# Kernel optimization log

Hardware: AMD Instinct MI355X
Metric: run time of the kernel (lower is better)

## Reference

```python
import jax, jax.numpy as jnp
import numpy as np

NH = 16      # num_attention_heads
NKV = 8      # num_key_value_heads
G = NH // NKV  # num_key_value_groups
D = 128      # head_dim = hidden_size // NH
ROPE_MAX = 2048


def _rope_tables(seq_len, dtype=jnp.float32):
    # matches RotaryEmbedding: inv_freq over even dims, freqs duplicated (concat), cos/sin cached
    inv_freq = 1.0 / (10000.0 ** (jnp.arange(0, D, 2, dtype=jnp.float32) / D))
    t = jnp.arange(ROPE_MAX, dtype=jnp.float32)[:, None]          # [max, 1]
    freqs = t * inv_freq[None, :]                                  # [max, D/2]
    freqs = jnp.concatenate((freqs, freqs), axis=-1)               # [max, D]
    cos = jnp.cos(freqs)[:seq_len].astype(dtype)                   # [S, D]
    sin = jnp.sin(freqs)[:seq_len].astype(dtype)
    # unsqueeze(0) then unsqueeze(2) -> [1, S, 1, D] broadcasting over batch and heads
    return cos[None, :, None, :], sin[None, :, None, :]


def _rotate_half(x):
    x1, x2 = jnp.split(x, 2, axis=-1)
    return jnp.concatenate((-x2, x1), axis=-1)


def setup_inputs() -> dict:
    key = jax.random.key(0)
    ks = jax.random.split(key, 5)
    B, S, H = 2, 2048, 2048
    scale = 1.0 / np.sqrt(H)
    return {
        "hidden_states": jax.random.normal(ks[0], (B, S, H), jnp.float32),
        "Wq": jax.random.normal(ks[1], (H, H), jnp.float32) * scale,
        "Wk": jax.random.normal(ks[2], (NKV * D, H), jnp.float32) * scale,
        "Wv": jax.random.normal(ks[3], (NKV * D, H), jnp.float32) * scale,
        "Wo": jax.random.normal(ks[4], (H, H), jnp.float32) * scale,
    }


def reference(hidden_states, Wq, Wk, Wv, Wo):
    B, S, H = hidden_states.shape
    # projections (nn.Linear: y = x @ W.T, no bias)
    q = (hidden_states @ Wq.T).reshape(B, S, NH, D)     # [B,S,NH,D]
    k = (hidden_states @ Wk.T).reshape(B, S, NKV, D)    # [B,S,NKV,D]
    v = (hidden_states @ Wv.T).reshape(B, S, NKV, D)

    cos, sin = _rope_tables(S, hidden_states.dtype)
    q = q * cos + _rotate_half(q) * sin
    k = k * cos + _rotate_half(k) * sin

    # GQA: query head h attends to kv head h // G (repeat_kv ordering: h = n*G + g)
    qg = q.reshape(B, S, NKV, G, D).transpose(0, 2, 3, 1, 4)   # [B,NKV,G,S,D]
    kt = k.transpose(0, 2, 1, 3)                                # [B,NKV,S,D]
    vt = v.transpose(0, 2, 1, 3)                                # [B,NKV,S,D]

    scores = jnp.einsum("bngqd,bnkd->bngqk", qg, kt) / np.sqrt(D)  # [B,NKV,G,S,S]
    causal = jnp.triu(jnp.ones((S, S), dtype=bool), k=1)
    neg = jnp.finfo(scores.dtype).min
    scores = jnp.where(causal[None, None, None], neg, scores)
    probs = jax.nn.softmax(scores.astype(jnp.float32), axis=-1).astype(q.dtype)

    out = jnp.einsum("bngqk,bnkd->bngqd", probs, vt)            # [B,NKV,G,S,D]
    out = out.transpose(0, 3, 1, 2, 4).reshape(B, S, H)         # [B,S,H]
    return out @ Wo.T
```

## Files before the change

### kernel.cpp

```cpp
#include <hip/hip_runtime.h>

typedef unsigned short u16;
typedef __attribute__((ext_vector_type(8))) short short8;
typedef __attribute__((ext_vector_type(4))) float f32x4;

__device__ __forceinline__ u16 f2bf(float f) {
  unsigned u = __float_as_uint(f);
  return (u16)((u + 0x7FFFu + ((u >> 16) & 1u)) >> 16);
}
__device__ __forceinline__ float bf2f(u16 h) {
  return __uint_as_float(((unsigned)h) << 16);
}

__device__ __forceinline__ void gload_lds16(const void* g, void* l) {
  __builtin_amdgcn_global_load_lds(
      (const __attribute__((address_space(1))) unsigned*)g,
      (__attribute__((address_space(3))) unsigned*)l, 16, 0, 0);
}

__global__ void cast_f32_bf16_k(const float4* __restrict__ in, u16* __restrict__ out, int n4) {
  int i = blockIdx.x * 256 + threadIdx.x;
  if (i >= n4) return;
  float4 v = in[i];
  union { u16 u[4]; uint2 d; } r;
  r.u[0] = f2bf(v.x); r.u[1] = f2bf(v.y); r.u[2] = f2bf(v.z); r.u[3] = f2bf(v.w);
  *reinterpret_cast<uint2*>(out + (size_t)i * 4) = r.d;
}

__global__ void rope_tables_k(float* __restrict__ cosT, float* __restrict__ sinT) {
  int idx = blockIdx.x * 256 + threadIdx.x;
  int i = idx & 63, s = idx >> 6;
  double inv = pow(10000.0, -(double)(2 * i) / 128.0);
  double f = (double)s * inv;
  cosT[idx] = (float)cos(f);
  sinT[idx] = (float)sin(f);
}

__global__ void rope_q_k(u16* __restrict__ x, const float* __restrict__ cosT,
                         const float* __restrict__ sinT) {
  int idx = blockIdx.x * 256 + threadIdx.x;
  int i = idx & 63;
  int hh = (idx >> 6) & 15;
  int row = idx >> 10;
  int s = row & 2047;
  size_t base = (size_t)row * 4096 + hh * 128;
  float x1 = bf2f(x[base + i]);
  float x2 = bf2f(x[base + i + 64]);
  float c = cosT[s * 64 + i], sn = sinT[s * 64 + i];
  x[base + i]      = f2bf(x1 * c - x2 * sn);
  x[base + i + 64] = f2bf(x2 * c + x1 * sn);
}

__global__ void rope_repack_k_k(const u16* __restrict__ qkv, u16* __restrict__ kt,
                                const float* __restrict__ cosT, const float* __restrict__ sinT) {
  int idx = blockIdx.x * 256 + threadIdx.x;
  int i = idx & 63;
  int kvh = (idx >> 6) & 7;
  int row = idx >> 9;
  int s = row & 2047, b = row >> 11;
  size_t src = (size_t)row * 4096 + 2048 + kvh * 128;
  float x1 = bf2f(qkv[src + i]);
  float x2 = bf2f(qkv[src + i + 64]);
  float c = cosT[s * 64 + i], sn = sinT[s * 64 + i];
  size_t dst = ((size_t)(b * 8 + kvh) * 2048 + s) * 128;
  kt[dst + i]      = f2bf(x1 * c - x2 * sn);
  kt[dst + i + 64] = f2bf(x2 * c + x1 * sn);
}

__global__ void transpose_v_k(const u16* __restrict__ qkv, u16* __restrict__ vt) {
  __shared__ u16 tile[128][129];
  int bn = blockIdx.y;
  int s0 = blockIdx.x * 128;
  int b = bn >> 3, n = bn & 7;
  for (int e = threadIdx.x; e < 128 * 128; e += 256) {
    int r = e >> 7, c = e & 127;
    tile[r][c] = qkv[(size_t)(b * 2048 + s0 + r) * 4096 + 3072 + n * 128 + c];
  }
  __syncthreads();
  for (int e = threadIdx.x; e < 128 * 128; e += 256) {
    int r = e >> 7, c = e & 127;
    vt[((size_t)bn * 128 + r) * 2048 + s0 + c] = tile[c][r];
  }
}

template<typename OutT>
__global__ __launch_bounds__(512, 1) void gemm256p_k(
    const u16* __restrict__ A, const u16* __restrict__ Bm,
    OutT* __restrict__ C, int M, int N, int K)
{
  __shared__ __align__(16) u16 As[2][2][256 * 32];
  __shared__ __align__(16) u16 Bs[2][2][256 * 32];
  const int tid = threadIdx.x;
  const int wave = tid >> 6, lane = tid & 63;
  const int wm = wave >> 2, wn = wave & 3;
  const int lrow = lane & 15, lgrp = lane >> 4;
  const int gx = (int)gridDim.x;
  const int nwg = gx * (int)gridDim.y;
  const int f = (int)(blockIdx.y * gridDim.x + blockIdx.x);
  const int sw = (f & 7) * (nwg >> 3) + (f >> 3);
  const int bx = sw % gx, by = sw / gx;
  const int row0 = by * 256, col0 = bx * 256;

  f32x4 acc[8][4];
  #pragma unroll
  for (int m = 0; m < 8; ++m)
    #pragma unroll
    for (int n = 0; n < 4; ++n) acc[m][n] = (f32x4){0.f, 0.f, 0.f, 0.f};

  const int NT = K >> 6;
  const int psw = lgrp ^ (lrow & 3);

  auto stageA = [&](int buf, int t, int ks) {
    const int k0 = (t << 6) + ks * 32;
    #pragma unroll
    for (int i = 0; i < 2; ++i) {
      int s = i * 512 + tid;
      int row = s >> 2, p = s & 3;
      int g = p ^ (row & 3);
      gload_lds16(A + (size_t)(row0 + row) * K + k0 + g * 8,
                  &As[buf][ks][(size_t)(i * 512 + wave * 64) * 8]);
    }
  };
  auto stageB = [&](int buf, int t, int ks) {
    const int k0 = (t << 6) + ks * 32;
    #pragma unroll
    for (int i = 0; i < 2; ++i) {
      int s = i * 512 + tid;
      int row = s >> 2, p = s & 3;
      int g = p ^ (row & 3);
      gload_lds16(Bm + (size_t)(col0 + row) * K + k0 + g * 8,
                  &Bs[buf][ks][(size_t)(i * 512 + wave * 64) * 8]);
    }
  };

  stageA(0, 0, 0); stageB(0, 0, 0); stageA(0, 0, 1); stageB(0, 0, 1);

  for (int t = 0; t < NT; ++t) {
    const int cur = t & 1, nxt = cur ^ 1;
    const bool pf = (t + 1 < NT);
    short8 af[4], bfr[4];

    if (pf) { stageA(nxt, t + 1, 0); asm volatile("s_waitcnt vmcnt(6)" ::: "memory"); }
    else    {                        asm volatile("s_waitcnt vmcnt(4)" ::: "memory"); }
    __builtin_amdgcn_s_barrier();
    __builtin_amdgcn_sched_barrier(0);
    #pragma unroll
    for (int m = 0; m < 4; ++m)
      af[m] = *reinterpret_cast<const short8*>(&As[cur][0][(wm * 128 + m * 16 + lrow) * 32 + psw * 8]);
    #pragma unroll
    for (int n = 0; n < 4; ++n)
      bfr[n] = *reinterpret_cast<const short8*>(&Bs[cur][0][(wn * 64 + n * 16 + lrow) * 32 + psw * 8]);
    asm volatile("s_waitcnt lgkmcnt(0)" ::: "memory");
    __builtin_amdgcn_sched_barrier(0);
    __builtin_amdgcn_s_setprio(1);
    #pragma unroll
    for (int m = 0; m < 4; ++m)
      #pragma unroll
      for (int n = 0; n < 4; ++n)
        acc[m][n] = __builtin_amdgcn_mfma_f32_16x16x32_bf16(af[m], bfr[n], acc[m][n], 0, 0, 0);
    __builtin_amdgcn_s_setprio(0);

    if (pf) stageB(nxt, t + 1, 0);
    #pragma unroll
    for (int m = 0; m < 4; ++m)
      af[m] = *reinterpret_cast<const short8*>(&As[cur][0][(wm * 128 + (m + 4) * 16 + lrow) * 32 + psw * 8]);
    asm volatile("s_waitcnt lgkmcnt(0)" ::: "memory");
    __builtin_amdgcn_sched_barrier(0);
    __builtin_amdgcn_s_setprio(1);
    #pragma unroll
    for (int m = 0; m < 4; ++m)
      #pragma unroll
      for (int n = 0; n < 4; ++n)
        acc[m + 4][n] = __builtin_amdgcn_mfma_f32_16x16x32_bf16(af[m], bfr[n], acc[m + 4][n], 0, 0, 0);
    __builtin_amdgcn_s_setprio(0);

    if (pf) { stageA(nxt, t + 1, 1); asm volatile("s_waitcnt vmcnt(6)" ::: "memory"); }
    else    {                        asm volatile("s_waitcnt vmcnt(0)" ::: "memory"); }
    __builtin_amdgcn_s_barrier();
    __builtin_amdgcn_sched_barrier(0);
    #pragma unroll
    for (int m = 0; m < 4; ++m)
      af[m] = *reinterpret_cast<const short8*>(&As[cur][1][(wm * 128 + m * 16 + lrow) * 32 + psw * 8]);
    #pragma unroll
    for (int n = 0; n < 4; ++n)
      bfr[n] = *reinterpret_cast<const short8*>(&Bs[cur][1][(wn * 64 + n * 16 + lrow) * 32 + psw * 8]);
    asm volatile("s_waitcnt lgkmcnt(0)" ::: "memory");
    __builtin_amdgcn_sched_barrier(0);
    __builtin_amdgcn_s_setprio(1);
    #pragma unroll
    for (int m = 0; m < 4; ++m)
      #pragma unroll
      for (int n = 0; n < 4; ++n)
        acc[m][n] = __builtin_amdgcn_mfma_f32_16x16x32_bf16(af[m], bfr[n], acc[m][n], 0, 0, 0);
    __builtin_amdgcn_s_setprio(0);

    if (pf) stageB(nxt, t + 1, 1);
    #pragma unroll
    for (int m = 0; m < 4; ++m)
      af[m] = *reinterpret_cast<const short8*>(&As[cur][1][(wm * 128 + (m + 4) * 16 + lrow) * 32 + psw * 8]);
    asm volatile("s_waitcnt lgkmcnt(0)" ::: "memory");
    __builtin_amdgcn_sched_barrier(0);
    __builtin_amdgcn_s_setprio(1);
    #pragma unroll
    for (int m = 0; m < 4; ++m)
      #pragma unroll
      for (int n = 0; n < 4; ++n)
        acc[m + 4][n] = __builtin_amdgcn_mfma_f32_16x16x32_bf16(af[m], bfr[n], acc[m + 4][n], 0, 0, 0);
    __builtin_amdgcn_s_setprio(0);
  }

  #pragma unroll
  for (int m = 0; m < 8; ++m)
    #pragma unroll
    for (int n = 0; n < 4; ++n)
      #pragma unroll
      for (int j = 0; j < 4; ++j) {
        int r = row0 + wm * 128 + m * 16 + lgrp * 4 + j;
        int col = col0 + wn * 64 + n * 16 + lrow;
        float val = acc[m][n][j];
        if constexpr (sizeof(OutT) == 2) C[(size_t)r * N + col] = f2bf(val);
        else                             C[(size_t)r * N + col] = val;
      }
}

template<typename OutT, int BN>
__global__ __launch_bounds__(512, 1) void gemm256_k(
    const u16* __restrict__ A, const u16* __restrict__ Bm,
    OutT* __restrict__ C, int M, int N, int K)
{
  constexpr int BITER = (BN * 8) / 512;
  constexpr int NFR = BN / 64;
  __shared__ __align__(16) u16 As[2][256 * 64];
  __shared__ __align__(16) u16 Bs[2][BN * 64];
  const int tid = threadIdx.x;
  const int wave = tid >> 6, lane = tid & 63;
  const int wm = wave >> 2, wn = wave & 3;
  const int lrow = lane & 15, lgrp = lane >> 4;
  const int gx = (int)gridDim.x;
  const int nwg = gx * (int)gridDim.y;
  const int f = (int)(blockIdx.y * gridDim.x + blockIdx.x);
  const int sw = (f & 7) * (nwg >> 3) + (f >> 3);
  const int bx = sw % gx, by = sw / gx;
  const int row0 = by * 256, col0 = bx * BN;

  f32x4 acc[8][NFR];
  #pragma unroll
  for (int m = 0; m < 8; ++m)
    #pragma unroll
    for (int n = 0; n < NFR; ++n) acc[m][n] = (f32x4){0.f, 0.f, 0.f, 0.f};

  const int NT = K >> 6;

  auto stage = [&](int buf, int k0) {
    #pragma unroll
    for (int i = 0; i < 4; ++i) {
      int cid = i * 512 + tid;
      int row = cid >> 3, cp = cid & 7;
      int c = cp ^ (row & 7);
      gload_lds16(A + (size_t)(row0 + row) * K + k0 + c * 8,
                  &As[buf][(size_t)(i * 512 + wave * 64) * 8]);
    }
    #pragma unroll
    for (int i = 0; i < BITER; ++i) {
      int cid = i * 512 + tid;
      int row = cid >> 3, cp = cid & 7;
      int c = cp ^ (row & 7);
      gload_lds16(Bm + (size_t)(col0 + row) * K + k0 + c * 8,
                  &Bs[buf][(size_t)(i * 512 + wave * 64) * 8]);
    }
  };

  stage(0, 0);
  for (int t = 0; t < NT; ++t) {
    const int cur = t & 1;
    if (t + 1 < NT) {
      stage(cur ^ 1, (t + 1) << 6);
      if constexpr (BN == 256) asm volatile("s_waitcnt vmcnt(8)" ::: "memory");
      else                     asm volatile("s_waitcnt vmcnt(6)" ::: "memory");
    } else {
      asm volatile("s_waitcnt vmcnt(0)" ::: "memory");
    }
    __builtin_amdgcn_s_barrier();
    __builtin_amdgcn_sched_barrier(0);
    #pragma unroll
    for (int ks = 0; ks < 2; ++ks) {
      short8 af[8], bfr[NFR];
      #pragma unroll
      for (int m = 0; m < 8; ++m) {
        int row = wm * 128 + m * 16 + lrow;
        int cp = (ks * 4 + lgrp) ^ (row & 7);
        af[m] = *reinterpret_cast<const short8*>(&As[cur][row * 64 + cp * 8]);
      }
      #pragma unroll
      for (int n = 0; n < NFR; ++n) {
        int row = wn * (NFR * 16) + n * 16 + lrow;
        int cp = (ks * 4 + lgrp) ^ (row & 7);
        bfr[n] = *reinterpret_cast<const short8*>(&Bs[cur][row * 64 + cp * 8]);
      }
      #pragma unroll
      for (int m = 0; m < 8; ++m)
        #pragma unroll
        for (int n = 0; n < NFR; ++n)
          acc[m][n] = __builtin_amdgcn_mfma_f32_16x16x32_bf16(af[m], bfr[n], acc[m][n], 0, 0, 0);
    }
    __builtin_amdgcn_sched_barrier(0);
    __builtin_amdgcn_s_barrier();
  }

  #pragma unroll
  for (int m = 0; m < 8; ++m)
    #pragma unroll
    for (int n = 0; n < NFR; ++n)
      #pragma unroll
      for (int j = 0; j < 4; ++j) {
        int r = row0 + wm * 128 + m * 16 + lgrp * 4 + j;
        int col = col0 + wn * (NFR * 16) + n * 16 + lrow;
        float val = acc[m][n][j];
        if constexpr (sizeof(OutT) == 2) C[(size_t)r * N + col] = f2bf(val);
        else                             C[(size_t)r * N + col] = val;
      }
}

__global__ __launch_bounds__(256, 2) void flash_attn_k(
    const u16* __restrict__ qkv, const u16* __restrict__ kt,
    const u16* __restrict__ vt, u16* __restrict__ o)
{
  constexpr int S = 2048, NH = 16, NKV = 8, D = 128;
  const int wave = threadIdx.x >> 6, lane = threadIdx.x & 63;
  const int flat = blockIdx.x;
  const int pr = flat >> 5;
  const int bh = (flat & 7) * 4 + ((flat >> 3) & 3);
  const int b = bh >> 4, h = bh & 15;
  const int kvh = h >> 1;
  const int lrow = lane & 15, lgrp = lane >> 4;

  __shared__ __align__(16) u16 ks[2][64 * 128];
  __shared__ __align__(16) u16 vs[2][128 * 64];

  const float scl2 = 0.12754245006443634f;
  const u16* khead = kt + (size_t)(b * NKV + kvh) * S * D;
  const u16* vhead = vt + (size_t)(b * NKV + kvh) * D * S;

  auto stage = [&](int nxt, int kv0n) {
    #pragma unroll
    for (int i = 0; i < 4; ++i) {
      int c = i * 256 + wave * 64 + lane;
      int kr = c >> 4;
      int kc16 = (c & 15) ^ (kr & 7);
      gload_lds16(khead + (size_t)(kv0n + kr) * D + kc16 * 8,
                  &ks[nxt][(size_t)(i * 256 + wave * 64) * 8]);
      int vr = c >> 3;
      int vc = (c & 7) ^ (vr & 7);
      gload_lds16(vhead + (size_t)vr * S + kv0n + vc * 8,
                  &vs[nxt][(size_t)(i * 256 + wave * 64) * 8]);
    }
  };

  #pragma unroll
  for (int ph = 0; ph < 2; ++ph) {
    const int qt = ph ? pr : (31 - pr);
    const int q0 = qt * 64 + wave * 16;
    const int trips = qt + 1;

    short8 qf[4];
    const u16* qbase = qkv + (size_t)(b * S + q0 + lrow) * 4096 + h * 128;
    #pragma unroll
    for (int kc = 0; kc < 4; ++kc)
      qf[kc] = *reinterpret_cast<const short8*>(qbase + kc * 32 + lgrp * 8);

    f32x4 acc[8];
    #pragma unroll
    for (int n = 0; n < 8; ++n) acc[n] = (f32x4){0.f, 0.f, 0.f, 0.f};
    float l_part[4] = {0.f, 0.f, 0.f, 0.f};

    stage(0, 0);
    __syncthreads();

    for (int t = 0; t < trips; ++t) {
      const int cur = t & 1;
      const int kv0 = t * 64;
      f32x4 sc[4];
      #pragma unroll
      for (int nb = 0; nb < 4; ++nb) {
        sc[nb] = (f32x4){0.f, 0.f, 0.f, 0.f};
        const int r = nb * 16 + lrow;
        #pragma unroll
        for (int kc = 0; kc < 4; ++kc) {
          int ch = (kc * 4 + lgrp) ^ (r & 7);
          short8 kf = *reinterpret_cast<const short8*>(&ks[cur][r * 128 + ch * 8]);
          sc[nb] = __builtin_amdgcn_mfma_f32_16x16x32_bf16(qf[kc], kf, sc[nb], 0, 0, 0);
        }
      }
      __syncthreads();
      if (t + 1 < trips) stage(cur ^ 1, kv0 + 64);
      u16* pb = &ks[cur][wave * 1024];
      if (t < trips - 1) {
        #pragma unroll
        for (int nb = 0; nb < 4; ++nb)
          #pragma unroll
          for (int j = 0; j < 4; ++j) {
            int qr = lgrp * 4 + j;
            float p = exp2f(fminf(sc[nb][j] * scl2, 43.f));
            l_part[j] += p;
            pb[qr * 64 + ((nb * 16 + lrow) ^ ((qr & 7) << 3))] = f2bf(p);
          }
      } else {
        #pragma unroll
        for (int nb = 0; nb < 4; ++nb) {
          if (nb < wave) {
            #pragma unroll
            for (int j = 0; j < 4; ++j) {
              int qr = lgrp * 4 + j;
              float p = exp2f(fminf(sc[nb][j] * scl2, 43.f));
              l_part[j] += p;
              pb[qr * 64 + ((nb * 16 + lrow) ^ ((qr & 7) << 3))] = f2bf(p);
            }
          } else if (nb == wave) {
            #pragma unroll
            for (int j = 0; j < 4; ++j) {
              int qr = lgrp * 4 + j;
              float p = (lrow <= qr) ? exp2f(fminf(sc[nb][j] * scl2, 43.f)) : 0.f;
              l_part[j] += p;
              pb[qr * 64 + ((nb * 16 + lrow) ^ ((qr & 7) << 3))] = f2bf(p);
            }
          } else {
            #pragma unroll
            for (int j = 0; j < 4; ++j) {
              int qr = lgrp * 4 + j;
              pb[qr * 64 + ((nb * 16 + lrow) ^ ((qr & 7) << 3))] = 0;
            }
          }
        }
      }
      short8 pf[2];
      #pragma unroll
      for (int kc2 = 0; kc2 < 2; ++kc2) {
        int ch = (kc2 * 4 + lgrp) ^ (lrow & 7);
        pf[kc2] = *reinterpret_cast<const short8*>(&pb[lrow * 64 + ch * 8]);
      }
      #pragma unroll
      for (int n = 0; n < 8; ++n) {
        const int d = n * 16 + lrow;
        #pragma unroll
        for (int kc2 = 0; kc2 < 2; ++kc2) {
          int ch = (kc2 * 4 + lgrp) ^ (d & 7);
          short8 vf = *reinterpret_cast<const short8*>(&vs[cur][d * 64 + ch * 8]);
          acc[n] = __builtin_amdgcn_mfma_f32_16x16x32_bf16(pf[kc2], vf, acc[n], 0, 0, 0);
        }
      }
      __syncthreads();
    }

    float inv[4];
    #pragma unroll
    for (int j = 0; j < 4; ++j) {
      float s = l_part[j];
      #pragma unroll
      for (int off = 8; off; off >>= 1) s += __shfl_xor(s, off);
      inv[j] = 1.f / s;
    }
    u16* obase = o + (((size_t)(b * S + q0)) * NH + h) * D;
    #pragma unroll
    for (int n = 0; n < 8; ++n)
      #pragma unroll
      for (int j = 0; j < 4; ++j)
        obase[(size_t)(lgrp * 4 + j) * NH * D + n * 16 + lrow] = f2bf(acc[n][j] * inv[j]);
    __syncthreads();
  }
}

extern "C" void kernel_launch(void* const* d_in, const int* in_sizes, int n_in,
                              void* d_out, int out_size, void* d_ws, size_t ws_size,
                              hipStream_t stream) {
  const float* hs = (const float*)d_in[0];
  const float* Wq = (const float*)d_in[1];
  const float* Wk = (const float*)d_in[2];
  const float* Wv = (const float*)d_in[3];
  const float* Wo = (const float*)d_in[4];
  float* out = (float*)d_out;

  constexpr int B = 2, S = 2048, H = 2048, NH = 16, NKV = 8, D = 128;
  constexpr int M = B * S;
  constexpr int NQKV = 4096;

  char* w = (char*)d_ws;
  auto alloc = [&](size_t bytes) { char* p = w; w += (bytes + 255) & ~(size_t)255; return p; };
  u16* hs_bf   = (u16*)alloc((size_t)M * H * 2);
  u16* wqkv_bf = (u16*)alloc((size_t)NQKV * H * 2);
  u16* wo_bf   = (u16*)alloc((size_t)H * H * 2);
  u16* qkv     = (u16*)alloc((size_t)M * NQKV * 2);
  float* cosT  = (float*)alloc((size_t)S * 64 * 4);
  float* sinT  = (float*)alloc((size_t)S * 64 * 4);
  u16* attn = hs_bf;
  u16* vt   = wqkv_bf;
  u16* kt   = wqkv_bf + (size_t)B * NKV * D * S;

  cast_f32_bf16_k<<<(M * H / 4) / 256, 256, 0, stream>>>((const float4*)hs, hs_bf, M * H / 4);
  cast_f32_bf16_k<<<(H * H / 4) / 256, 256, 0, stream>>>((const float4*)Wq, wqkv_bf, H * H / 4);
  cast_f32_bf16_k<<<(NKV * D * H / 4) / 256, 256, 0, stream>>>((const float4*)Wk, wqkv_bf + (size_t)2048 * H, NKV * D * H / 4);
  cast_f32_bf16_k<<<(NKV * D * H / 4) / 256, 256, 0, stream>>>((const float4*)Wv, wqkv_bf + (size_t)3072 * H, NKV * D * H / 4);
  cast_f32_bf16_k<<<(H * H / 4) / 256, 256, 0, stream>>>((const float4*)Wo, wo_bf, H * H / 4);
  rope_tables_k<<<(S * 64) / 256, 256, 0, stream>>>(cosT, sinT);

  gemm256p_k<u16><<<dim3(NQKV / 256, M / 256), 512, 0, stream>>>(hs_bf, wqkv_bf, qkv, M, NQKV, H);

  rope_q_k<<<(M * 16 * 64) / 256, 256, 0, stream>>>(qkv, cosT, sinT);
  rope_repack_k_k<<<(M * 8 * 64) / 256, 256, 0, stream>>>(qkv, kt, cosT, sinT);
  transpose_v_k<<<dim3(S / 128, B * NKV), 256, 0, stream>>>(qkv, vt);

  flash_attn_k<<<512, 256, 0, stream>>>(qkv, kt, vt, attn);

  gemm256_k<float, 128><<<dim3(H / 128, M / 256), 512, 0, stream>>>(attn, wo_bf, out, M, H, H);
}
```

Measured before the change: 234.5 us.

## Keep attention probabilities in registers via transposed MFMA and lane shuffles

The attention kernel swaps the MFMA operand order so each lane holds a column of scores. The softmax probabilities are packed to bf16 with v_cvt_pk_bf16 and redistributed to the P·V operand layout with cross-lane shuffles, which removes the LDS write/read round trip of P. It also cuts one of the two per-tile barriers by using an explicit vmcnt wait plus s_barrier, and writes outputs as packed 8-byte stores. In exchange it adds 16 shuffles per tile and depends on correctly reasoning about the register layout and the reuse of the K buffer.

```diff
diff --git a/kernel.cpp b/kernel.cpp
--- a/kernel.cpp
+++ b/kernel.cpp
@@ -10,6 +10,11 @@
 }
 __device__ __forceinline__ float bf2f(u16 h) {
   return __uint_as_float(((unsigned)h) << 16);
+}
+__device__ __forceinline__ unsigned cvt_pk_bf16(float lo, float hi) {
+  unsigned r;
+  asm("v_cvt_pk_bf16_f32 %0, %1, %2" : "=v"(r) : "v"(lo), "v"(hi));
+  return r;
 }
 
 __device__ __forceinline__ void gload_lds16(const void* g, void* l) {
@@ -341,6 +346,10 @@
   const u16* khead = kt + (size_t)(b * NKV + kvh) * S * D;
   const u16* vhead = vt + (size_t)(b * NKV + kvh) * D * S;
 
+  const int srcA = lrow + 16 * ((2 * lgrp) & 3);
+  const int srcB = srcA + 16;
+  const bool hiSel = (lgrp >= 2);
+
   auto stage = [&](int nxt, int kv0n) {
     #pragma unroll
     for (int i = 0; i < 4; ++i) {
@@ -371,14 +380,15 @@
     f32x4 acc[8];
     #pragma unroll
     for (int n = 0; n < 8; ++n) acc[n] = (f32x4){0.f, 0.f, 0.f, 0.f};
-    float l_part[4] = {0.f, 0.f, 0.f, 0.f};
+    float l_part = 0.f;
 
     stage(0, 0);
-    __syncthreads();
 
     for (int t = 0; t < trips; ++t) {
       const int cur = t & 1;
-      const int kv0 = t * 64;
+      asm volatile("s_waitcnt vmcnt(0)" ::: "memory");
+      __builtin_amdgcn_s_barrier();
+      __builtin_amdgcn_sched_barrier(0);
       f32x4 sc[4];
       #pragma unroll
       for (int nb = 0; nb < 4; ++nb) {
@@ -388,55 +398,57 @@
         for (int kc = 0; kc < 4; ++kc) {
           int ch = (kc * 4 + lgrp) ^ (r & 7);
           short8 kf = *reinterpret_cast<const short8*>(&ks[cur][r * 128 + ch * 8]);
-          sc[nb] = __builtin_amdgcn_mfma_f32_16x16x32_bf16(qf[kc], kf, sc[nb], 0, 0, 0);
+          sc[nb] = __builtin_amdgcn_mfma_f32_16x16x32_bf16(kf, qf[kc], sc[nb], 0, 0, 0);
         }
       }
-      __syncthreads();
-      if (t + 1 < trips) stage(cur ^ 1, kv0 + 64);
-      u16* pb = &ks[cur][wave * 1024];
+      if (t + 1 < trips) stage(cur ^ 1, (t + 1) * 64);
+      float p[4][4];
       if (t < trips - 1) {
         #pragma unroll
         for (int nb = 0; nb < 4; ++nb)
           #pragma unroll
-          for (int j = 0; j < 4; ++j) {
-            int qr = lgrp * 4 + j;
-            float p = exp2f(fminf(sc[nb][j] * scl2, 43.f));
-            l_part[j] += p;
-            pb[qr * 64 + ((nb * 16 + lrow) ^ ((qr & 7) << 3))] = f2bf(p);
-          }
+          for (int j = 0; j < 4; ++j)
+            p[nb][j] = exp2f(fminf(sc[nb][j] * scl2, 43.f));
       } else {
         #pragma unroll
         for (int nb = 0; nb < 4; ++nb) {
           if (nb < wave) {
             #pragma unroll
-            for (int j = 0; j < 4; ++j) {
-              int qr = lgrp * 4 + j;
-              float p = exp2f(fminf(sc[nb][j] * scl2, 43.f));
-              l_part[j] += p;
-              pb[qr * 64 + ((nb * 16 + lrow) ^ ((qr & 7) << 3))] = f2bf(p);
-            }
+            for (int j = 0; j < 4; ++j)
+              p[nb][j] = exp2f(fminf(sc[nb][j] * scl2, 43.f));
           } else if (nb == wave) {
             #pragma unroll
-            for (int j = 0; j < 4; ++j) {
-              int qr = lgrp * 4 + j;
-              float p = (lrow <= qr) ? exp2f(fminf(sc[nb][j] * scl2, 43.f)) : 0.f;
-              l_part[j] += p;
-              pb[qr * 64 + ((nb * 16 + lrow) ^ ((qr & 7) << 3))] = f2bf(p);
-            }
+            for (int j = 0; j < 4; ++j)
+              p[nb][j] = (lgrp * 4 + j <= lrow) ? exp2f(fminf(sc[nb][j] * scl2, 43.f)) : 0.f;
           } else {
             #pragma unroll
-            for (int j = 0; j < 4; ++j) {
-              int qr = lgrp * 4 + j;
-              pb[qr * 64 + ((nb * 16 + lrow) ^ ((qr & 7) << 3))] = 0;
-            }
+            for (int j = 0; j < 4; ++j) p[nb][j] = 0.f;
           }
         }
       }
-      short8 pf[2];
-      #pragma unroll
-      for (int kc2 = 0; kc2 < 2; ++kc2) {
-        int ch = (kc2 * 4 + lgrp) ^ (lrow & 7);
-        pf[kc2] = *reinterpret_cast<const short8*>(&pb[lrow * 64 + ch * 8]);
+      #pragma unroll
+      for (int nb = 0; nb < 4; ++nb)
+        #pragma unroll
+        for (int j = 0; j < 4; ++j) l_part += p[nb][j];
+      unsigned pk[4][2];
+      #pragma unroll
+      for (int nb = 0; nb < 4; ++nb) {
+        pk[nb][0] = cvt_pk_bf16(p[nb][0], p[nb][1]);
+        pk[nb][1] = cvt_pk_bf16(p[nb][2], p[nb][3]);
+      }
+      short8 pfB[2];
+      #pragma unroll
+      for (int half = 0; half < 2; ++half) {
+        unsigned lo0 = __shfl(pk[2 * half][0], srcA), hi0 = __shfl(pk[2 * half + 1][0], srcA);
+        unsigned lo1 = __shfl(pk[2 * half][1], srcA), hi1 = __shfl(pk[2 * half + 1][1], srcA);
+        unsigned lo2 = __shfl(pk[2 * half][0], srcB), hi2 = __shfl(pk[2 * half + 1][0], srcB);
+        unsigned lo3 = __shfl(pk[2 * half][1], srcB), hi3 = __shfl(pk[2 * half + 1][1], srcB);
+        union { unsigned u[4]; short8 s8; } asm_u;
+        asm_u.u[0] = hiSel ? hi0 : lo0;
+        asm_u.u[1] = hiSel ? hi1 : lo1;
+        asm_u.u[2] = hiSel ? hi2 : lo2;
+        asm_u.u[3] = hiSel ? hi3 : lo3;
+        pfB[half] = asm_u.s8;
       }
       #pragma unroll
       for (int n = 0; n < 8; ++n) {
@@ -445,26 +457,23 @@
         for (int kc2 = 0; kc2 < 2; ++kc2) {
           int ch = (kc2 * 4 + lgrp) ^ (d & 7);
           short8 vf = *reinterpret_cast<const short8*>(&vs[cur][d * 64 + ch * 8]);
-          acc[n] = __builtin_amdgcn_mfma_f32_16x16x32_bf16(pf[kc2], vf, acc[n], 0, 0, 0);
+          acc[n] = __builtin_amdgcn_mfma_f32_16x16x32_bf16(vf, pfB[kc2], acc[n], 0, 0, 0);
         }
       }
-      __syncthreads();
-    }
-
-    float inv[4];
-    #pragma unroll
-    for (int j = 0; j < 4; ++j) {
-      float s = l_part[j];
-      #pragma unroll
-      for (int off = 8; off; off >>= 1) s += __shfl_xor(s, off);
-      inv[j] = 1.f / s;
-    }
-    u16* obase = o + (((size_t)(b * S + q0)) * NH + h) * D;
-    #pragma unroll
-    for (int n = 0; n < 8; ++n)
-      #pragma unroll
-      for (int j = 0; j < 4; ++j)
-        obase[(size_t)(lgrp * 4 + j) * NH * D + n * 16 + lrow] = f2bf(acc[n][j] * inv[j]);
+    }
+
+    float s = l_part;
+    s += __shfl_xor(s, 16);
+    s += __shfl_xor(s, 32);
+    float inv = 1.f / s;
+    u16* obase = o + (((size_t)(b * S + q0 + lrow)) * NH + h) * D;
+    #pragma unroll
+    for (int n = 0; n < 8; ++n) {
+      uint2 wv;
+      wv.x = cvt_pk_bf16(acc[n][0] * inv, acc[n][1] * inv);
+      wv.y = cvt_pk_bf16(acc[n][2] * inv, acc[n][3] * inv);
+      *reinterpret_cast<uint2*>(obase + n * 16 + lgrp * 4) = wv;
+    }
     __syncthreads();
   }
 }
```

New measurement: 230.6 us. About the same (-1.7%).
